# Kernel optimization log

Hardware: AMD Instinct MI355X
Metric: run time of the kernel (lower is better)

## Reference

```python
import jax, jax.numpy as jnp
import numpy as np

jax.config.update("jax_enable_x64", True)

MANT_SCALE = 8388608.0  # 2**23


def _decode_fp32_bits(bits):
    """[..., 32] {0,1} pulses (MSB-first IEEE-754 float32) -> float64 value."""
    f64 = jnp.float64
    sign = 1.0 - 2.0 * bits[..., 0].astype(f64)
    e = jnp.einsum('...j,j->...', bits[..., 1:9].astype(f64),
                   jnp.exp2(jnp.arange(7, -1, -1, dtype=f64)))
    frac = jnp.einsum('...j,j->...', bits[..., 9:32].astype(f64),
                      jnp.exp2(-jnp.arange(1, 24, dtype=f64)))
    normal = sign * jnp.exp2(e - 127.0) * (1.0 + frac)
    subnorm = sign * jnp.exp2(-126.0) * frac
    return jnp.where(e > 0, normal, subnorm)


def _encode_fp32_bits(y):
    """float64 value already on the fp32 grid -> [..., 32] {0,1} pulses (MSB-first)."""
    f64 = jnp.float64
    sbit = (y < 0).astype(f64)
    a = jnp.abs(y)
    e = jnp.clip(jnp.floor(jnp.log2(jnp.where(a > 0, a, 1.0))), -126.0, 127.0)
    eb = jnp.where(a > 0, e + 127.0, 0.0)          # biased exponent, 0 for zero/subnormal
    frac = jnp.where(eb > 0, a * jnp.exp2(-e) - 1.0, a * jnp.exp2(126.0))
    mant = frac * MANT_SCALE                        # exact integer for fp32-grid y
    ebits = jnp.mod(jnp.floor(eb[..., None] * jnp.exp2(-jnp.arange(7, -1, -1, dtype=f64))), 2.0)
    mbits = jnp.mod(jnp.floor(mant[..., None] * jnp.exp2(-jnp.arange(22, -1, -1, dtype=f64))), 2.0)
    bits = jnp.concatenate([sbit[..., None], ebits, mbits], axis=-1)
    return jnp.where((a > 0)[..., None], bits, 0.0).astype(jnp.float32)


def setup_inputs() -> dict:
    rng = np.random.default_rng(0)
    vals = (rng.standard_normal((1, 2048, 1024)) * 2.0).astype(np.float32)
    words = vals.view(np.uint32)
    shifts = np.arange(31, -1, -1, dtype=np.uint32)
    bits = ((words[..., None] >> shifts) & np.uint32(1)).astype(np.float32)
    return {"x": jnp.asarray(bits)}


def reference(x):
    # GELU(x) ~= x * sigmoid(1.702 * x), all intermediates in fp64 (as the
    # gate-level pipeline does), final result rounded once to fp32 bits.
    xv = _decode_fp32_bits(x)
    y64 = xv * jax.nn.sigmoid(1.702 * xv)
    y32 = y64.astype(jnp.float32).astype(jnp.float64)  # FP64 -> FP32 rounding
    return _encode_fp32_bits(y32)
```

## Files before the change

### kernel.cpp

```cpp
#include <hip/hip_runtime.h>
#include <math.h>


#define LN2C 0x1.62e42fefa39efp-1

typedef unsigned int u32x4 __attribute__((ext_vector_type(4)));

__global__ __launch_bounds__(256) void build_tables(double* __restrict__ dt,
                                                    uint32_t* __restrict__ et) {
#pragma clang fp contract(off)
  const double LN2 = LN2C;
  __shared__ double Wdec[8], Lms[23];
  const int t = threadIdx.x;
  if (t < 8) Wdec[t] = exp((double)(7 - t) * LN2);
  if (t >= 31 && t < 54) Lms[t - 31] = exp((double)(31 - t) * LN2);
  __syncthreads();

  if (t == 0) {
    dt[0] = exp(-126.0 * LN2);
    et[0] = 0u;
  } else {
    double e_c = 0.0;
#pragma unroll
    for (int j = 0; j < 8; ++j)
      if ((t >> (7 - j)) & 1) e_c = e_c + Wdec[j];
    dt[t] = exp((e_c - 127.0) * LN2);
  }
  if (t < 23) dt[256 + t] = exp((double)(-1 - t) * LN2);
  if (t < 23) dt[279 + t] = Lms[t];
  if (t < 254) {
    double e0 = (double)(t - 126);
    dt[302 + t] = exp(-e0 * LN2);
  }
  if (t >= 1 && t < 255) {
    double eb = (double)t;
    uint32_t r = 0;
#pragma unroll
    for (int sc = 7; sc >= 0; --sc) {
      double f = floor(eb * Lms[sc]);
      double md = f - 2.0 * floor(0.5 * f);
      r |= ((uint32_t)md) << (23 + sc);
    }
    et[t] = r;
  }
}

__global__ __launch_bounds__(256) void spike_gelu_kernel(
    const u32x4* __restrict__ in, u32x4* __restrict__ out,
    const double* __restrict__ dt, const uint32_t* __restrict__ et,
    int n_vals) {
#pragma clang fp contract(off)
  const double LN2 = LN2C;
  __shared__ double dtab[556];
  __shared__ uint32_t etab[256];
  __shared__ uint32_t lds_w[512];

  const int tid = threadIdx.x;
  for (int i = tid; i < 556; i += 256) dtab[i] = dt[i];
  etab[tid] = et[tid];

  const int n_chunks = n_vals * 8;
  const int blk_chunk0 = blockIdx.x * 4096;

  const int nibshift = 28 - 4 * (tid & 7);
#pragma unroll
  for (int i = 0; i < 8; ++i) {
    int g0 = blk_chunk0 + i * 256 + tid;
    int g1 = g0 + 2048;
    uint32_t nib0 = 0, nib1 = 0;
    if (g0 < n_chunks) {
      u32x4 b = __builtin_nontemporal_load(&in[g0]);
      nib0 = (((b.x >> 23) & 1u) << 3) | (((b.y >> 23) & 1u) << 2) |
             (((b.z >> 23) & 1u) << 1) | ((b.w >> 23) & 1u);
    }
    if (g1 < n_chunks) {
      u32x4 b = __builtin_nontemporal_load(&in[g1]);
      nib1 = (((b.x >> 23) & 1u) << 3) | (((b.y >> 23) & 1u) << 2) |
             (((b.z >> 23) & 1u) << 1) | ((b.w >> 23) & 1u);
    }
    uint32_t p0 = nib0 << nibshift, p1 = nib1 << nibshift;
    p0 |= __shfl_xor(p0, 1);  p1 |= __shfl_xor(p1, 1);
    p0 |= __shfl_xor(p0, 2);  p1 |= __shfl_xor(p1, 2);
    p0 |= __shfl_xor(p0, 4);  p1 |= __shfl_xor(p1, 4);
    if ((tid & 7) == 0) {
      lds_w[i * 32 + (tid >> 3)] = p0;
      lds_w[256 + i * 32 + (tid >> 3)] = p1;
    }
  }
  __syncthreads();

  const int v0 = blockIdx.x * 512 + tid;
  const int v1 = v0 + 256;
  const bool ok0 = v0 < n_vals, ok1 = v1 < n_vals;
  const uint32_t w0 = lds_w[tid], w1 = lds_w[256 + tid];
  const double* E1t  = dtab;
  const double* Vdec = dtab + 256;
  const double* Lm   = dtab + 279;
  const double* P2t  = dtab + 302;

  double f0 = 0.0, f1 = 0.0;
#pragma unroll
  for (int j = 0; j < 23; ++j) {
    double vj = Vdec[j];
    if ((w0 >> (22 - j)) & 1u) f0 = f0 + vj;
    if ((w1 >> (22 - j)) & 1u) f1 = f1 + vj;
  }
  uint32_t ei0 = (w0 >> 23) & 0xFFu, ei1 = (w1 >> 23) & 0xFFu;
  double sg0 = (w0 >> 31) ? -1.0 : 1.0, sg1 = (w1 >> 31) ? -1.0 : 1.0;
  double fa0 = ei0 ? (1.0 + f0) : f0, fa1 = ei1 ? (1.0 + f1) : f1;
  double x0 = (sg0 * E1t[ei0]) * fa0, x1 = (sg1 * E1t[ei1]) * fa1;

  double t0 = 1.702 * x0, t1 = 1.702 * x1;
  double e0v = exp(-t0), e1v = exp(-t1);
  double s0 = 1.0 / (1.0 + e0v), s1 = 1.0 / (1.0 + e1v);
  double y0 = x0 * s0, y1 = x1 * s1;
  float yf0 = (float)y0, yf1 = (float)y1;
  double yd0 = (double)yf0, yd1 = (double)yf1;

  double a0 = fabs(yd0), a1 = fabs(yd1);
  uint32_t yb0 = __float_as_uint(yf0), yb1 = __float_as_uint(yf1);
  uint32_t Ef0 = (yb0 >> 23) & 0xFFu, Ef1 = (yb1 >> 23) & 0xFFu;
  uint32_t mbf0 = yb0 & 0x7FFFFFu, mbf1 = yb1 & 0x7FFFFFu;
  int e00 = (Ef0 == 0u) ? -126 : (int)Ef0 - 127;
  int e01 = (Ef1 == 0u) ? -126 : (int)Ef1 - 127;
  bool pw0 = ok0 && (a0 > 0.0) && (Ef0 != 0u) && (mbf0 == 0u);
  bool pw1 = ok1 && (a1 > 0.0) && (Ef1 != 0u) && (mbf1 == 0u);
  if (__builtin_expect(pw0 || pw1, 0)) {
    if (pw0) {
      double e0 = floor(log(a0) / LN2);
      e00 = (int)fmin(fmax(e0, -126.0), 127.0);
    }
    if (pw1) {
      double e0 = floor(log(a1) / LN2);
      e01 = (int)fmin(fmax(e0, -126.0), 127.0);
    }
  }
  double p20 = P2t[e00 + 126], p21 = P2t[e01 + 126];
  double m10 = a0 * p20, m11 = a1 * p21;
  double mant0 = (m10 - 1.0) * 8388608.0;
  double mant1 = (m11 - 1.0) * 8388608.0;
  int M0 = (int)rint(mant0), M1 = (int)rint(mant1);
  uint32_t mb0 = ((uint32_t)M0) & 0x7FFFFFu, mb1 = ((uint32_t)M1) & 0x7FFFFFu;
  int T0 = M0 ? __builtin_ctz((uint32_t)M0) : 23;
  int T1 = M1 ? __builtin_ctz((uint32_t)M1) : 23;
  int L0 = T0 < 22 ? T0 : 22, L1 = T1 < 22 ? T1 : 22;
  int Lmax = L0 > L1 ? L0 : L1;
  for (int sc = 0; sc <= Lmax; ++sc) {
    double lm = Lm[sc];
    if (sc <= L0) {
      double f = floor(mant0 * lm);
      mb0 = (mb0 & ~(1u << sc)) | (((uint32_t)(((int)f) & 1)) << sc);
    }
    if (sc <= L1) {
      double f = floor(mant1 * lm);
      mb1 = (mb1 & ~(1u << sc)) | (((uint32_t)(((int)f) & 1)) << sc);
    }
  }
  uint32_t ob0 = (yb0 & 0x80000000u) | etab[e00 + 127] | mb0;
  uint32_t ob1 = (yb1 & 0x80000000u) | etab[e01 + 127] | mb1;
  ob0 = (ok0 && a0 > 0.0) ? ob0 : 0u;
  ob1 = (ok1 && a1 > 0.0) ? ob1 : 0u;

  lds_w[tid] = ob0;
  lds_w[256 + tid] = ob1;
  __syncthreads();

#pragma unroll
  for (int i = 0; i < 8; ++i) {
    int g0 = blk_chunk0 + i * 256 + tid;
    int g1 = g0 + 2048;
    int base = 31 - 4 * (tid & 7);
    uint32_t wv0 = lds_w[i * 32 + (tid >> 3)];
    uint32_t wv1 = lds_w[256 + i * 32 + (tid >> 3)];
    if (g0 < n_chunks) {
      u32x4 o;
      o.x = ((wv0 >> base) & 1u) * 0x3F800000u;
      o.y = ((wv0 >> (base - 1)) & 1u) * 0x3F800000u;
      o.z = ((wv0 >> (base - 2)) & 1u) * 0x3F800000u;
      o.w = ((wv0 >> (base - 3)) & 1u) * 0x3F800000u;
      __builtin_nontemporal_store(o, &out[g0]);
    }
    if (g1 < n_chunks) {
      u32x4 o;
      o.x = ((wv1 >> base) & 1u) * 0x3F800000u;
      o.y = ((wv1 >> (base - 1)) & 1u) * 0x3F800000u;
      o.z = ((wv1 >> (base - 2)) & 1u) * 0x3F800000u;
      o.w = ((wv1 >> (base - 3)) & 1u) * 0x3F800000u;
      __builtin_nontemporal_store(o, &out[g1]);
    }
  }
}

extern "C" void kernel_launch(void* const* d_in, const int* in_sizes, int n_in,
                              void* d_out, int out_size, void* d_ws, size_t ws_size,
                              hipStream_t stream) {
  int n_vals = in_sizes[0] / 32;
  double* dt = (double*)d_ws;
  uint32_t* et = (uint32_t*)((char*)d_ws + 556 * sizeof(double));
  build_tables<<<1, 256, 0, stream>>>(dt, et);
  int grid = (n_vals + 511) / 512;
  spike_gelu_kernel<<<grid, 256, 0, stream>>>(
      (const u32x4*)d_in[0], (u32x4*)d_out, dt, et, n_vals);
}
```

Baseline: 426.2 us.

## Fuse table build into main kernel and regroup values per wavefront

```diff
diff --git a/kernel.cpp b/kernel.cpp
--- a/kernel.cpp
+++ b/kernel.cpp
@@ -6,34 +6,48 @@
 
 typedef unsigned int u32x4 __attribute__((ext_vector_type(4)));
 
-__global__ __launch_bounds__(256) void build_tables(double* __restrict__ dt,
-                                                    uint32_t* __restrict__ et) {
+__global__ __launch_bounds__(256) void spike_gelu_kernel(
+    const u32x4* __restrict__ in, u32x4* __restrict__ out, int n_vals) {
 #pragma clang fp contract(off)
   const double LN2 = LN2C;
-  __shared__ double Wdec[8], Lms[23];
-  const int t = threadIdx.x;
-  if (t < 8) Wdec[t] = exp((double)(7 - t) * LN2);
-  if (t >= 31 && t < 54) Lms[t - 31] = exp((double)(31 - t) * LN2);
+  __shared__ double Wdec[8];
+  __shared__ double Lms[23];
+  __shared__ double E1t[256];
+  __shared__ double Vdec[23];
+  __shared__ double P2t[254];
+  __shared__ uint32_t etab[256];
+
+  const int tid = threadIdx.x;
+  if (tid < 8) Wdec[tid] = exp((double)(7 - tid) * LN2);
+  if (tid >= 31 && tid < 54) Lms[tid - 31] = exp((double)(31 - tid) * LN2);
   __syncthreads();
 
-  if (t == 0) {
-    dt[0] = exp(-126.0 * LN2);
-    et[0] = 0u;
+  const int lane = tid & 63;
+  const int vbase = blockIdx.x * 512 + (tid >> 6) * 128;
+  const int n_chunks = n_vals * 8;
+  const int cbase = vbase * 8 + lane;
+  u32x4 bufA[8];
+#pragma unroll
+  for (int i = 0; i < 8; ++i) {
+    int g = cbase + i * 64;
+    u32x4 b = {0u, 0u, 0u, 0u};
+    if (g < n_chunks) b = __builtin_nontemporal_load(&in[g]);
+    bufA[i] = b;
+  }
+
+  if (tid == 0) {
+    E1t[0] = exp(-126.0 * LN2);
   } else {
     double e_c = 0.0;
 #pragma unroll
     for (int j = 0; j < 8; ++j)
-      if ((t >> (7 - j)) & 1) e_c = e_c + Wdec[j];
-    dt[t] = exp((e_c - 127.0) * LN2);
-  }
-  if (t < 23) dt[256 + t] = exp((double)(-1 - t) * LN2);
-  if (t < 23) dt[279 + t] = Lms[t];
-  if (t < 254) {
-    double e0 = (double)(t - 126);
-    dt[302 + t] = exp(-e0 * LN2);
-  }
-  if (t >= 1 && t < 255) {
-    double eb = (double)t;
+      if ((tid >> (7 - j)) & 1) e_c = e_c + Wdec[j];
+    E1t[tid] = exp((e_c - 127.0) * LN2);
+  }
+  if (tid < 23) Vdec[tid] = exp((double)(-1 - tid) * LN2);
+  if (tid < 254) P2t[tid] = exp((double)(126 - tid) * LN2);
+  if (tid >= 1 && tid < 255) {
+    double eb = (double)tid;
     uint32_t r = 0;
 #pragma unroll
     for (int sc = 7; sc >= 0; --sc) {
@@ -41,62 +55,50 @@
       double md = f - 2.0 * floor(0.5 * f);
       r |= ((uint32_t)md) << (23 + sc);
     }
-    et[t] = r;
-  }
-}
-
-__global__ __launch_bounds__(256) void spike_gelu_kernel(
-    const u32x4* __restrict__ in, u32x4* __restrict__ out,
-    const double* __restrict__ dt, const uint32_t* __restrict__ et,
-    int n_vals) {
-#pragma clang fp contract(off)
-  const double LN2 = LN2C;
-  __shared__ double dtab[556];
-  __shared__ uint32_t etab[256];
-  __shared__ uint32_t lds_w[512];
-
-  const int tid = threadIdx.x;
-  for (int i = tid; i < 556; i += 256) dtab[i] = dt[i];
-  etab[tid] = et[tid];
-
-  const int n_chunks = n_vals * 8;
-  const int blk_chunk0 = blockIdx.x * 4096;
-
-  const int nibshift = 28 - 4 * (tid & 7);
-#pragma unroll
-  for (int i = 0; i < 8; ++i) {
-    int g0 = blk_chunk0 + i * 256 + tid;
-    int g1 = g0 + 2048;
-    uint32_t nib0 = 0, nib1 = 0;
-    if (g0 < n_chunks) {
-      u32x4 b = __builtin_nontemporal_load(&in[g0]);
-      nib0 = (((b.x >> 23) & 1u) << 3) | (((b.y >> 23) & 1u) << 2) |
-             (((b.z >> 23) & 1u) << 1) | ((b.w >> 23) & 1u);
-    }
-    if (g1 < n_chunks) {
-      u32x4 b = __builtin_nontemporal_load(&in[g1]);
-      nib1 = (((b.x >> 23) & 1u) << 3) | (((b.y >> 23) & 1u) << 2) |
-             (((b.z >> 23) & 1u) << 1) | ((b.w >> 23) & 1u);
-    }
-    uint32_t p0 = nib0 << nibshift, p1 = nib1 << nibshift;
-    p0 |= __shfl_xor(p0, 1);  p1 |= __shfl_xor(p1, 1);
-    p0 |= __shfl_xor(p0, 2);  p1 |= __shfl_xor(p1, 2);
-    p0 |= __shfl_xor(p0, 4);  p1 |= __shfl_xor(p1, 4);
-    if ((tid & 7) == 0) {
-      lds_w[i * 32 + (tid >> 3)] = p0;
-      lds_w[256 + i * 32 + (tid >> 3)] = p1;
-    }
+    etab[tid] = r;
+  } else {
+    etab[tid] = 0u;
   }
   __syncthreads();
 
-  const int v0 = blockIdx.x * 512 + tid;
-  const int v1 = v0 + 256;
+  u32x4 bufB[8];
+#pragma unroll
+  for (int i = 0; i < 8; ++i) {
+    int g = cbase + 512 + i * 64;
+    u32x4 b = {0u, 0u, 0u, 0u};
+    if (g < n_chunks) b = __builtin_nontemporal_load(&in[g]);
+    bufB[i] = b;
+  }
+
+  const int nibshift = 28 - 4 * (lane & 7);
+  const int keep = lane & 7;
+  uint32_t w0 = 0u, w1 = 0u;
+#pragma unroll
+  for (int i = 0; i < 8; ++i) {
+    u32x4 b = bufA[i];
+    uint32_t p = (((((b.x >> 23) & 1u) << 3) | (((b.y >> 23) & 1u) << 2) |
+                   (((b.z >> 23) & 1u) << 1) | ((b.w >> 23) & 1u)))
+                 << nibshift;
+    p |= __shfl_xor(p, 1);
+    p |= __shfl_xor(p, 2);
+    p |= __shfl_xor(p, 4);
+    if (keep == i) w0 = p;
+  }
+#pragma unroll
+  for (int i = 0; i < 8; ++i) {
+    u32x4 b = bufB[i];
+    uint32_t p = (((((b.x >> 23) & 1u) << 3) | (((b.y >> 23) & 1u) << 2) |
+                   (((b.z >> 23) & 1u) << 1) | ((b.w >> 23) & 1u)))
+                 << nibshift;
+    p |= __shfl_xor(p, 1);
+    p |= __shfl_xor(p, 2);
+    p |= __shfl_xor(p, 4);
+    if (keep == i) w1 = p;
+  }
+
+  const int v0 = vbase + (lane & 7) * 8 + (lane >> 3);
+  const int v1 = v0 + 64;
   const bool ok0 = v0 < n_vals, ok1 = v1 < n_vals;
-  const uint32_t w0 = lds_w[tid], w1 = lds_w[256 + tid];
-  const double* E1t  = dtab;
-  const double* Vdec = dtab + 256;
-  const double* Lm   = dtab + 279;
-  const double* P2t  = dtab + 302;
 
   double f0 = 0.0, f1 = 0.0;
 #pragma unroll
@@ -146,7 +148,7 @@
   int L0 = T0 < 22 ? T0 : 22, L1 = T1 < 22 ? T1 : 22;
   int Lmax = L0 > L1 ? L0 : L1;
   for (int sc = 0; sc <= Lmax; ++sc) {
-    double lm = Lm[sc];
+    double lm = Lms[sc];
     if (sc <= L0) {
       double f = floor(mant0 * lm);
       mb0 = (mb0 & ~(1u << sc)) | (((uint32_t)(((int)f) & 1)) << sc);
@@ -161,31 +163,28 @@
   ob0 = (ok0 && a0 > 0.0) ? ob0 : 0u;
   ob1 = (ok1 && a1 > 0.0) ? ob1 : 0u;
 
-  lds_w[tid] = ob0;
-  lds_w[256 + tid] = ob1;
-  __syncthreads();
-
-#pragma unroll
-  for (int i = 0; i < 8; ++i) {
-    int g0 = blk_chunk0 + i * 256 + tid;
-    int g1 = g0 + 2048;
-    int base = 31 - 4 * (tid & 7);
-    uint32_t wv0 = lds_w[i * 32 + (tid >> 3)];
-    uint32_t wv1 = lds_w[256 + i * 32 + (tid >> 3)];
+#pragma unroll
+  for (int i = 0; i < 8; ++i) {
+    int g0 = cbase + i * 64;
+    int g1 = g0 + 512;
+    int src = (lane & 56) + i;
+    uint32_t wa = __shfl(ob0, src);
+    uint32_t wb = __shfl(ob1, src);
+    int base = 31 - 4 * (lane & 7);
     if (g0 < n_chunks) {
       u32x4 o;
-      o.x = ((wv0 >> base) & 1u) * 0x3F800000u;
-      o.y = ((wv0 >> (base - 1)) & 1u) * 0x3F800000u;
-      o.z = ((wv0 >> (base - 2)) & 1u) * 0x3F800000u;
-      o.w = ((wv0 >> (base - 3)) & 1u) * 0x3F800000u;
+      o.x = ((wa >> base) & 1u) * 0x3F800000u;
+      o.y = ((wa >> (base - 1)) & 1u) * 0x3F800000u;
+      o.z = ((wa >> (base - 2)) & 1u) * 0x3F800000u;
+      o.w = ((wa >> (base - 3)) & 1u) * 0x3F800000u;
       __builtin_nontemporal_store(o, &out[g0]);
     }
     if (g1 < n_chunks) {
       u32x4 o;
-      o.x = ((wv1 >> base) & 1u) * 0x3F800000u;
-      o.y = ((wv1 >> (base - 1)) & 1u) * 0x3F800000u;
-      o.z = ((wv1 >> (base - 2)) & 1u) * 0x3F800000u;
-      o.w = ((wv1 >> (base - 3)) & 1u) * 0x3F800000u;
+      o.x = ((wb >> base) & 1u) * 0x3F800000u;
+      o.y = ((wb >> (base - 1)) & 1u) * 0x3F800000u;
+      o.z = ((wb >> (base - 2)) & 1u) * 0x3F800000u;
+      o.w = ((wb >> (base - 3)) & 1u) * 0x3F800000u;
       __builtin_nontemporal_store(o, &out[g1]);
     }
   }
@@ -195,10 +194,7 @@
                               void* d_out, int out_size, void* d_ws, size_t ws_size,
                               hipStream_t stream) {
   int n_vals = in_sizes[0] / 32;
-  double* dt = (double*)d_ws;
-  uint32_t* et = (uint32_t*)((char*)d_ws + 556 * sizeof(double));
-  build_tables<<<1, 256, 0, stream>>>(dt, et);
   int grid = (n_vals + 511) / 512;
   spike_gelu_kernel<<<grid, 256, 0, stream>>>(
-      (const u32x4*)d_in[0], (u32x4*)d_out, dt, et, n_vals);
+      (const u32x4*)d_in[0], (u32x4*)d_out, n_vals);
 }
```

Result: no change. 419.3 us (-1.6%).
